# Optimization experiments

Hardware: AMD Instinct MI355X
Metric: run time of the kernel (lower is better)

The kernel has to match this reference:

```python
import jax, jax.numpy as jnp
from jax import lax
import numpy as np

B = 262144
CLASSES = 11


def setup_inputs() -> dict:
    key = jax.random.key(0)
    ks = jax.random.split(key, 8)
    exponents = jax.random.randint(ks[0], (B, 16), 0, CLASSES, dtype=jnp.int32)
    conv0_w = jax.random.normal(ks[1], (4, 12, 1, 2), jnp.float32) * 0.1
    conv0_b = jax.random.normal(ks[2], (4,), jnp.float32) * 0.05
    conv1_w = jax.random.normal(ks[3], (4, 12, 2, 1), jnp.float32) * 0.1
    # xavier-uniform linears, bias filled with 0.01 (as in init_weights)
    lim1 = float(np.sqrt(6.0 / (96 + 256)))
    linear_w = jax.random.uniform(ks[4], (256, 96), jnp.float32, -lim1, lim1)
    linear_b = jnp.full((256,), 0.01, jnp.float32)
    lim2 = float(np.sqrt(6.0 / (256 + 4)))
    out_w = jax.random.uniform(ks[5], (4, 256), jnp.float32, -lim2, lim2)
    out_b = jnp.full((4,), 0.01, jnp.float32)
    return {"exponents": exponents, "conv0_w": conv0_w, "conv0_b": conv0_b,
            "conv1_w": conv1_w, "linear_w": linear_w, "linear_b": linear_b,
            "out_w": out_w, "out_b": out_b}


def _conv(x, w):
    return lax.conv_general_dilated(x, w, (1, 1), 'VALID',
                                    dimension_numbers=('NCHW', 'OIHW', 'NCHW'))


def _forward(exponents, conv0_w, conv0_b, conv1_w, linear_w, linear_b, out_w, out_b):
    e = exponents.reshape(-1, 4, 4)
    # reconstruct board values: 0 tile stays 0, else 2**e
    x = jnp.where(e == 0, 0.0, jnp.exp2(e.astype(jnp.float32)))  # [B,4,4]
    # rotate_normalize: flips chosen from argmax corner (computed BEFORE flipping)
    corners = jnp.stack([x[:, 0, 0], x[:, 0, -1], x[:, -1, 0], x[:, -1, -1]], axis=1)
    ix = jnp.argmax(corners, axis=1)
    flip_v = ix >= 2          # floor(ix/2) == 1
    flip_h = (ix % 2) == 1
    x = jnp.where(flip_v[:, None, None], x[:, ::-1, :], x)
    x = jnp.where(flip_h[:, None, None], x[:, :, ::-1], x)
    # log2 with 0 -> 0, one-hot over 11 classes
    x_log = jnp.log2(x + (x == 0).astype(jnp.float32))
    onehot = jax.nn.one_hot(jnp.round(x_log).astype(jnp.int32), CLASSES,
                            dtype=jnp.float32)          # [B,4,4,11]
    onehot = jnp.transpose(onehot, (0, 3, 1, 2))         # [B,11,4,4]
    mask = onehot.sum(axis=1, keepdims=True)             # channel 0 (all ones)
    feat = jnp.concatenate([mask, onehot], axis=1)       # [B,12,4,4]
    zh = jax.nn.relu(_conv(feat, conv0_w) + conv0_b[None, :, None, None])  # [B,4,4,3]
    zv = jax.nn.relu(_conv(feat, conv1_w))                                  # [B,4,3,4]
    z1 = jnp.concatenate([zh.reshape(-1, 48), zv.reshape(-1, 48)], axis=1)  # [B,96]
    z2 = jax.nn.relu(z1 @ linear_w.T + linear_b)                            # [B,256]
    probs = jax.nn.softmax(z2 @ out_w.T + out_b, axis=1)                    # [B,4]
    # unscramble: vert swaps actions (0,1); horiz swaps actions (2,3)
    perm = jnp.stack([jnp.where(flip_v, 1, 0), jnp.where(flip_v, 0, 1),
                      jnp.where(flip_h, 3, 2), jnp.where(flip_h, 2, 3)], axis=1)
    return jnp.take_along_axis(probs, perm, axis=1)


def reference(exponents, conv0_w, conv0_b, conv1_w, linear_w, linear_b, out_w, out_b):
    return _forward(exponents, conv0_w, conv0_b, conv1_w, linear_w, linear_b, out_w, out_b)
```

## Files before the change

### kernel.cpp

```cpp
#include <hip/hip_runtime.h>

typedef unsigned int  u32;
typedef unsigned short u16;

typedef float    f4  __attribute__((ext_vector_type(4)));
typedef short    bf8 __attribute__((ext_vector_type(8)));
typedef __fp16   h8  __attribute__((ext_vector_type(8)));
typedef __fp16   h2  __attribute__((ext_vector_type(2)));

#define NBLK  1024
#define ITERS 4
#define ZSTR  104
#define SSTR  104

__device__ __forceinline__ u32 bfr(float f) {
    union { float f; u32 u; } v; v.f = f;
    return (v.u + 0x7fffu + ((v.u >> 16) & 1u)) >> 16;
}
__device__ __forceinline__ u32 pk2(float lo, float hi) { return bfr(lo) | (bfr(hi) << 16); }
__device__ __forceinline__ float blo(u32 u) { union { u32 u; float f; } v; v.u = u << 16;        return v.f; }
__device__ __forceinline__ float bhi(u32 u) { union { u32 u; float f; } v; v.u = u & 0xffff0000u; return v.f; }
__device__ __forceinline__ u32 pkh(float lo, float hi) {
    union { h2 h; u32 u; } v; v.h = __builtin_amdgcn_cvt_pkrtz(lo, hi); return v.u;
}
__device__ __forceinline__ u32 nrev(u32 x) {
    return ((x >> 12) & 0xFu) | ((x >> 4) & 0xF0u) | ((x << 4) & 0xF00u) | ((x << 12) & 0xF000u);
}

__launch_bounds__(256, 4)
__global__ void smartcnn_fused(const int* __restrict__ exps,
                               const float* __restrict__ c0w, const float* __restrict__ c0b,
                               const float* __restrict__ c1w,
                               const float* __restrict__ lw,  const float* __restrict__ lb,
                               const float* __restrict__ ow,  const float* __restrict__ ob,
                               float* __restrict__ out)
{
    __shared__ uint2  ThA[121];
    __shared__ uint2  TvA[121];
    __shared__ u16    z1[64 * ZSTR];
    __shared__ u32    zs[4][16 * SSTR / 2];
    __shared__ float4 Pbuf[4][4][16];
    __shared__ u32    flg[64];

    const int tid  = threadIdx.x;
    const int w    = tid >> 6;
    const int lane = tid & 63;
    const int m    = lane & 15;
    const int qd   = lane >> 4;

    for (int i = tid; i < 121; i += 256) {
        int v1 = i / 11, v2 = i - v1 * 11;
        float hv[4], vv[4];
        #pragma unroll
        for (int c = 0; c < 4; ++c) {
            hv[c] = fmaxf(c0w[c*24 + 0] + c0w[c*24 + (1+v1)*2 + 0] + c0b[c]
                        + c0w[c*24 + 1] + c0w[c*24 + (1+v2)*2 + 1], 0.f);
            vv[c] = fmaxf(c1w[c*24 + 0] + c1w[c*24 + (1+v1)*2 + 0]
                        + c1w[c*24 + 1] + c1w[c*24 + (1+v2)*2 + 1], 0.f);
        }
        ThA[i] = make_uint2(pk2(hv[0], hv[1]), pk2(hv[2], hv[3]));
        TvA[i] = make_uint2(pk2(vv[0], vv[1]), pk2(vv[2], vv[3]));
    }

    bf8 af[4][3];
    {
        u16* srow = (u16*)&zs[w][0] + m * SSTR;
        #pragma unroll
        for (int tt = 0; tt < 4; ++tt) {
            const float* rowp = lw + (size_t)((w*4 + tt)*16 + m)*96 + qd*24;
            #pragma unroll
            for (int v = 0; v < 6; ++v) {
                float4 x = *(const float4*)(rowp + v*4);
                u16 e[4] = {(u16)bfr(x.x), (u16)bfr(x.y), (u16)bfr(x.z), (u16)bfr(x.w)};
                #pragma unroll
                for (int j = 0; j < 4; ++j) {
                    int ko = qd*24 + v*4 + j;
                    int kp = (ko < 48) ? ((ko % 12)*4 + ko/12)
                                       : (48 + ((ko - 48) % 12)*4 + (ko - 48)/12);
                    srow[kp] = e[j];
                }
            }
            #pragma unroll
            for (int s = 0; s < 3; ++s)
                af[tt][s] = *(const bf8*)(srow + s*32 + qd*8);
        }
    }
    u32 owA[2][4];
    #pragma unroll
    for (int c = 0; c < 2; ++c) {
        int n8 = 64*w + 32*c + qd*8;
        #pragma unroll
        for (int k = 0; k < 4; ++k)
            owA[c][k] = (m < 4) ? pkh(ow[m*256 + n8 + 2*k], ow[m*256 + n8 + 2*k + 1]) : 0u;
    }
    u32 lbp[4][2];
    #pragma unroll
    for (int tt = 0; tt < 4; ++tt) {
        int n0 = 64*w + 16*tt + qd*4;
        lbp[tt][0] = pk2(lb[n0+0], lb[n0+1]);
        lbp[tt][1] = pk2(lb[n0+2], lb[n0+3]);
    }
    const float4 obv = *(const float4*)ob;

    const int b0 = blockIdx.x * (ITERS * 64);
    __syncthreads();

    int4 e4 = *(const int4*)(exps + (size_t)(b0 + w*16 + m)*16 + qd*4);
    u32 fl = 0;

    #pragma unroll 1
    for (int it = 0; it < ITERS; ++it) {
        if (it > 0) {
            float4 s0 = Pbuf[qd][0][m], s1 = Pbuf[qd][1][m];
            float4 s2 = Pbuf[qd][2][m], s3 = Pbuf[qd][3][m];
            float L0 = s0.x + s1.x + s2.x + s3.x + obv.x;
            float L1 = s0.y + s1.y + s2.y + s3.y + obv.y;
            float L2 = s0.z + s1.z + s2.z + s3.z + obv.z;
            float L3 = s0.w + s1.w + s2.w + s3.w + obv.w;
            float mx = fmaxf(fmaxf(L0, L1), fmaxf(L2, L3));
            float e0 = __expf(L0 - mx), e1 = __expf(L1 - mx), e2 = __expf(L2 - mx), e3 = __expf(L3 - mx);
            float inv = 1.0f / (e0 + e1 + e2 + e3);
            float p0 = e0 * inv, p1 = e1 * inv, p2 = e2 * inv, p3 = e3 * inv;
            float4 o;
            o.x = (fl & 1u) ? p1 : p0;
            o.y = (fl & 1u) ? p0 : p1;
            o.z = (fl & 2u) ? p3 : p2;
            o.w = (fl & 2u) ? p2 : p3;
            *(float4*)(out + (size_t)(b0 + (it-1)*64 + qd*16 + m) * 4) = o;
        }

        {
            u32 pkd = (u32)e4.x | ((u32)e4.y << 4) | ((u32)e4.z << 8) | ((u32)e4.w << 12);
            u32 R0 = (u32)__shfl((int)pkd, m);
            u32 R1 = (u32)__shfl((int)pkd, m + 16);
            u32 R2 = (u32)__shfl((int)pkd, m + 32);
            u32 R3 = (u32)__shfl((int)pkd, m + 48);
            u32 c0v = R0 & 15u, c1v = (R0 >> 12) & 15u, c2v = R3 & 15u, c3v = (R3 >> 12) & 15u;
            u32 best = c0v; int ix = 0;
            if (c1v > best) { best = c1v; ix = 1; }
            if (c2v > best) { best = c2v; ix = 2; }
            if (c3v > best) { best = c3v; ix = 3; }
            const bool fv = (ix >= 2), fh = ((ix & 1) != 0);
            u32 F[4];
            F[0] = fv ? R3 : R0;
            F[1] = fv ? R2 : R1;
            F[2] = fv ? R1 : R2;
            F[3] = fv ? R0 : R3;
            #pragma unroll
            for (int i = 0; i < 4; ++i) F[i] = fh ? nrev(F[i]) : F[i];

            if (qd == 0) flg[w*16 + m] = (u32)fv | ((u32)fh << 1);

            const u32 Fq = F[qd];
            u32 nbq[4], nbc[4];
            #pragma unroll
            for (int j = 0; j < 4; ++j) nbq[j] = (Fq >> (4*j)) & 15u;
            #pragma unroll
            for (int i = 0; i < 4; ++i) nbc[i] = (F[i] >> (4*qd)) & 15u;

            uint2 H0 = ThA[nbq[0]*11u + nbq[1]];
            uint2 H1 = ThA[nbq[1]*11u + nbq[2]];
            uint2 H2 = ThA[nbq[2]*11u + nbq[3]];
            uint2 V0 = TvA[nbc[0]*11u + nbc[1]];
            uint2 V1 = TvA[nbc[1]*11u + nbc[2]];
            uint2 V2 = TvA[nbc[2]*11u + nbc[3]];

            u16* zrow = &z1[(w*16 + m) * ZSTR];
            *(uint2*)(zrow + (qd*3 + 0)*4) = H0;
            *(uint2*)(zrow + (qd*3 + 1)*4) = H1;
            *(uint2*)(zrow + (qd*3 + 2)*4) = H2;
            *(uint2*)(zrow + 48 + (0*4 + qd)*4) = V0;
            *(uint2*)(zrow + 48 + (1*4 + qd)*4) = V1;
            *(uint2*)(zrow + 48 + (2*4 + qd)*4) = V2;
        }

        if (it + 1 < ITERS)
            e4 = *(const int4*)(exps + (size_t)(b0 + (it+1)*64 + w*16 + m)*16 + qd*4);

        __syncthreads();

        fl = flg[qd*16 + m];

        u32* zw = &zs[w][0];
        const int laneA = (((2*qd)    ) & 3)*16 + m;
        const int laneB = (((2*qd) + 1) & 3)*16 + m;
        #pragma unroll
        for (int G = 0; G < 4; ++G) {
            bf8 zb[3];
            #pragma unroll
            for (int s = 0; s < 3; ++s)
                zb[s] = *(const bf8*)(&z1[(G*16 + m)*ZSTR + s*32 + qd*8]);

            f4 acc_t[4];
            #pragma unroll
            for (int tt = 0; tt < 4; ++tt) {
                f4 b;
                b[0] = blo(lbp[tt][0]); b[1] = bhi(lbp[tt][0]);
                b[2] = blo(lbp[tt][1]); b[3] = bhi(lbp[tt][1]);
                acc_t[tt] = b;
            }
            #pragma unroll
            for (int s = 0; s < 3; ++s)
                #pragma unroll
                for (int tt = 0; tt < 4; ++tt)
                    acc_t[tt] = __builtin_amdgcn_mfma_f32_16x16x32_bf16(af[tt][s], zb[s], acc_t[tt], 0, 0, 0);

            u32 z2p[8];
            #pragma unroll
            for (int tt = 0; tt < 4; ++tt) {
                z2p[tt*2+0] = pkh(fmaxf(acc_t[tt][0], 0.f), fmaxf(acc_t[tt][1], 0.f));
                z2p[tt*2+1] = pkh(fmaxf(acc_t[tt][2], 0.f), fmaxf(acc_t[tt][3], 0.f));
            }
            *(uint4*)&zw[lane*12 + 0] = make_uint4(z2p[0], z2p[1], z2p[2], z2p[3]);
            *(uint4*)&zw[lane*12 + 4] = make_uint4(z2p[4], z2p[5], z2p[6], z2p[7]);

            f4 acc2 = {0.f, 0.f, 0.f, 0.f};
            #pragma unroll
            for (int c = 0; c < 2; ++c) {
                const int tt = 2*c + (qd >> 1);
                uint2 uA = *(const uint2*)&zw[laneA*12 + tt*2];
                uint2 uB = *(const uint2*)&zw[laneB*12 + tt*2];
                union { u32 u[4]; h8 v; } bu, au;
                bu.u[0] = uA.x; bu.u[1] = uA.y; bu.u[2] = uB.x; bu.u[3] = uB.y;
                au.u[0] = owA[c][0]; au.u[1] = owA[c][1]; au.u[2] = owA[c][2]; au.u[3] = owA[c][3];
                acc2 = __builtin_amdgcn_mfma_f32_16x16x32_f16(au.v, bu.v, acc2, 0, 0, 0);
            }
            if (qd == 0)
                Pbuf[G][w][m] = make_float4(acc2[0], acc2[1], acc2[2], acc2[3]);
        }
        __syncthreads();
    }

    {
        float4 s0 = Pbuf[qd][0][m], s1 = Pbuf[qd][1][m];
        float4 s2 = Pbuf[qd][2][m], s3 = Pbuf[qd][3][m];
        float L0 = s0.x + s1.x + s2.x + s3.x + obv.x;
        float L1 = s0.y + s1.y + s2.y + s3.y + obv.y;
        float L2 = s0.z + s1.z + s2.z + s3.z + obv.z;
        float L3 = s0.w + s1.w + s2.w + s3.w + obv.w;
        float mx = fmaxf(fmaxf(L0, L1), fmaxf(L2, L3));
        float e0 = __expf(L0 - mx), e1 = __expf(L1 - mx), e2 = __expf(L2 - mx), e3 = __expf(L3 - mx);
        float inv = 1.0f / (e0 + e1 + e2 + e3);
        float p0 = e0 * inv, p1 = e1 * inv, p2 = e2 * inv, p3 = e3 * inv;
        float4 o;
        o.x = (fl & 1u) ? p1 : p0;
        o.y = (fl & 1u) ? p0 : p1;
        o.z = (fl & 2u) ? p3 : p2;
        o.w = (fl & 2u) ? p2 : p3;
        *(float4*)(out + (size_t)(b0 + (ITERS-1)*64 + qd*16 + m) * 4) = o;
    }
}

extern "C" void kernel_launch(void* const* d_in, const int* in_sizes, int n_in,
                              void* d_out, int out_size, void* d_ws, size_t ws_size,
                              hipStream_t stream) {
    const int*   exps = (const int*)  d_in[0];
    const float* c0w  = (const float*)d_in[1];
    const float* c0b  = (const float*)d_in[2];
    const float* c1w  = (const float*)d_in[3];
    const float* lw   = (const float*)d_in[4];
    const float* lbv  = (const float*)d_in[5];
    const float* oww  = (const float*)d_in[6];
    const float* obv  = (const float*)d_in[7];
    smartcnn_fused<<<NBLK, 256, 0, stream>>>(exps, c0w, c0b, c1w, lw, lbv, oww, obv, (float*)d_out);
}
```

Baseline: 105.4 us.

## Switch to grid-stride chunk loop with 1280 blocks and fp32 bias init

Replaces the fixed four-chunks-per-block schedule with a grid-stride loop over 4096 chunks of 64 samples, launched as 1280 blocks, to change load balance across CUs and the tail. The second-layer bias is kept as fp32 float4 vectors instead of packed bf16 values that were unpacked on every iteration. Weight staging now reuses the z1 buffer and zs is resized. The 4096/1280 split leaves some blocks with one more chunk than others.

New measurement: 117.6 us. 11.6% more time.

```diff
diff --git a/kernel.cpp b/kernel.cpp
--- a/kernel.cpp
+++ b/kernel.cpp
@@ -8,18 +8,15 @@
 typedef __fp16   h8  __attribute__((ext_vector_type(8)));
 typedef __fp16   h2  __attribute__((ext_vector_type(2)));
 
-#define NBLK  1024
-#define ITERS 4
-#define ZSTR  104
-#define SSTR  104
+#define NBLK   1280
+#define NCHUNK 4096
+#define ZSTR   104
 
 __device__ __forceinline__ u32 bfr(float f) {
     union { float f; u32 u; } v; v.f = f;
     return (v.u + 0x7fffu + ((v.u >> 16) & 1u)) >> 16;
 }
 __device__ __forceinline__ u32 pk2(float lo, float hi) { return bfr(lo) | (bfr(hi) << 16); }
-__device__ __forceinline__ float blo(u32 u) { union { u32 u; float f; } v; v.u = u << 16;        return v.f; }
-__device__ __forceinline__ float bhi(u32 u) { union { u32 u; float f; } v; v.u = u & 0xffff0000u; return v.f; }
 __device__ __forceinline__ u32 pkh(float lo, float hi) {
     union { h2 h; u32 u; } v; v.h = __builtin_amdgcn_cvt_pkrtz(lo, hi); return v.u;
 }
@@ -38,7 +35,7 @@
     __shared__ uint2  ThA[121];
     __shared__ uint2  TvA[121];
     __shared__ u16    z1[64 * ZSTR];
-    __shared__ u32    zs[4][16 * SSTR / 2];
+    __shared__ u32    zs[4][64 * 12];
     __shared__ float4 Pbuf[4][4][16];
     __shared__ u32    flg[64];
 
@@ -64,7 +61,7 @@
 
     bf8 af[4][3];
     {
-        u16* srow = (u16*)&zs[w][0] + m * SSTR;
+        u16* srow = &z1[(w*16 + m) * ZSTR];
         #pragma unroll
         for (int tt = 0; tt < 4; ++tt) {
             const float* rowp = lw + (size_t)((w*4 + tt)*16 + m)*96 + qd*24;
@@ -93,24 +90,24 @@
         for (int k = 0; k < 4; ++k)
             owA[c][k] = (m < 4) ? pkh(ow[m*256 + n8 + 2*k], ow[m*256 + n8 + 2*k + 1]) : 0u;
     }
-    u32 lbp[4][2];
+    f4 lb4[4];
     #pragma unroll
-    for (int tt = 0; tt < 4; ++tt) {
-        int n0 = 64*w + 16*tt + qd*4;
-        lbp[tt][0] = pk2(lb[n0+0], lb[n0+1]);
-        lbp[tt][1] = pk2(lb[n0+2], lb[n0+3]);
-    }
+    for (int tt = 0; tt < 4; ++tt)
+        lb4[tt] = *(const f4*)(lb + 64*w + 16*tt + qd*4);
     const float4 obv = *(const float4*)ob;
 
-    const int b0 = blockIdx.x * (ITERS * 64);
     __syncthreads();
 
-    int4 e4 = *(const int4*)(exps + (size_t)(b0 + w*16 + m)*16 + qd*4);
+    int bi = blockIdx.x;
+    int4 e4 = *(const int4*)(exps + (size_t)(bi*64 + w*16 + m)*16 + qd*4);
     u32 fl = 0;
+    int pb = -1;
 
     #pragma unroll 1
-    for (int it = 0; it < ITERS; ++it) {
-        if (it > 0) {
+    for (; bi < NCHUNK; bi += NBLK) {
+        const int b0 = bi * 64;
+
+        if (pb >= 0) {
             float4 s0 = Pbuf[qd][0][m], s1 = Pbuf[qd][1][m];
             float4 s2 = Pbuf[qd][2][m], s3 = Pbuf[qd][3][m];
             float L0 = s0.x + s1.x + s2.x + s3.x + obv.x;
@@ -126,7 +123,7 @@
             o.y = (fl & 1u) ? p0 : p1;
             o.z = (fl & 2u) ? p3 : p2;
             o.w = (fl & 2u) ? p2 : p3;
-            *(float4*)(out + (size_t)(b0 + (it-1)*64 + qd*16 + m) * 4) = o;
+            *(float4*)(out + (size_t)(pb + qd*16 + m) * 4) = o;
         }
 
         {
@@ -174,12 +171,13 @@
             *(uint2*)(zrow + 48 + (2*4 + qd)*4) = V2;
         }
 
-        if (it + 1 < ITERS)
-            e4 = *(const int4*)(exps + (size_t)(b0 + (it+1)*64 + w*16 + m)*16 + qd*4);
+        if (bi + NBLK < NCHUNK)
+            e4 = *(const int4*)(exps + (size_t)((bi + NBLK)*64 + w*16 + m)*16 + qd*4);
 
         __syncthreads();
 
         fl = flg[qd*16 + m];
+        pb = b0;
 
         u32* zw = &zs[w][0];
         const int laneA = (((2*qd)    ) & 3)*16 + m;
@@ -191,14 +189,7 @@
             for (int s = 0; s < 3; ++s)
                 zb[s] = *(const bf8*)(&z1[(G*16 + m)*ZSTR + s*32 + qd*8]);
 
-            f4 acc_t[4];
-            #pragma unroll
-            for (int tt = 0; tt < 4; ++tt) {
-                f4 b;
-                b[0] = blo(lbp[tt][0]); b[1] = bhi(lbp[tt][0]);
-                b[2] = blo(lbp[tt][1]); b[3] = bhi(lbp[tt][1]);
-                acc_t[tt] = b;
-            }
+            f4 acc_t[4] = {lb4[0], lb4[1], lb4[2], lb4[3]};
             #pragma unroll
             for (int s = 0; s < 3; ++s)
                 #pragma unroll
@@ -231,7 +222,7 @@
         __syncthreads();
     }
 
-    {
+    if (pb >= 0) {
         float4 s0 = Pbuf[qd][0][m], s1 = Pbuf[qd][1][m];
         float4 s2 = Pbuf[qd][2][m], s3 = Pbuf[qd][3][m];
         float L0 = s0.x + s1.x + s2.x + s3.x + obv.x;
@@ -247,7 +238,7 @@
         o.y = (fl & 1u) ? p0 : p1;
         o.z = (fl & 2u) ? p3 : p2;
         o.w = (fl & 2u) ? p2 : p3;
-        *(float4*)(out + (size_t)(b0 + (ITERS-1)*64 + qd*16 + m) * 4) = o;
+        *(float4*)(out + (size_t)(pb + qd*16 + m) * 4) = o;
     }
 }
 
```

## Permute linear weight rows so MFMA outputs feed second MFMA directly in registers

Applied to the files above, without the earlier changes.

The order of the linear-layer output features assigned to each MFMA tile is permuted, both for the weight rows and for the bias. With that order, the accumulator layout of the first bf16 MFMA matches the operand layout the second f16 MFMA expects. This removes the per-group shared-memory round trip (write z2, read it back through lane shuffles) and the separate zs scratch buffer, and the bias is kept as fp32 vectors instead of bf16-packed values. It relies on the permuted feature order lining up exactly with the output-weight packing.

Result: no change. 104.0 us (-1.3%).

```diff
diff --git a/kernel.cpp b/kernel.cpp
--- a/kernel.cpp
+++ b/kernel.cpp
@@ -11,15 +11,12 @@
 #define NBLK  1024
 #define ITERS 4
 #define ZSTR  104
-#define SSTR  104
 
 __device__ __forceinline__ u32 bfr(float f) {
     union { float f; u32 u; } v; v.f = f;
     return (v.u + 0x7fffu + ((v.u >> 16) & 1u)) >> 16;
 }
 __device__ __forceinline__ u32 pk2(float lo, float hi) { return bfr(lo) | (bfr(hi) << 16); }
-__device__ __forceinline__ float blo(u32 u) { union { u32 u; float f; } v; v.u = u << 16;        return v.f; }
-__device__ __forceinline__ float bhi(u32 u) { union { u32 u; float f; } v; v.u = u & 0xffff0000u; return v.f; }
 __device__ __forceinline__ u32 pkh(float lo, float hi) {
     union { h2 h; u32 u; } v; v.h = __builtin_amdgcn_cvt_pkrtz(lo, hi); return v.u;
 }
@@ -38,7 +35,6 @@
     __shared__ uint2  ThA[121];
     __shared__ uint2  TvA[121];
     __shared__ u16    z1[64 * ZSTR];
-    __shared__ u32    zs[4][16 * SSTR / 2];
     __shared__ float4 Pbuf[4][4][16];
     __shared__ u32    flg[64];
 
@@ -48,6 +44,7 @@
     const int m    = lane & 15;
     const int qd   = lane >> 4;
 
+
     for (int i = tid; i < 121; i += 256) {
         int v1 = i / 11, v2 = i - v1 * 11;
         float hv[4], vv[4];
@@ -64,10 +61,12 @@
 
     bf8 af[4][3];
     {
-        u16* srow = (u16*)&zs[w][0] + m * SSTR;
+        u16* srow = &z1[(w*16 + m) * ZSTR];
         #pragma unroll
         for (int tt = 0; tt < 4; ++tt) {
-            const float* rowp = lw + (size_t)((w*4 + tt)*16 + m)*96 + qd*24;
+            const int tbase = ((tt & 1) ? 4 : 0) + ((tt >> 1) ? 32 : 0);
+            const int fid = 64*w + tbase + 8*(m >> 2) + (m & 3);
+            const float* rowp = lw + (size_t)fid*96 + qd*24;
             #pragma unroll
             for (int v = 0; v < 6; ++v) {
                 float4 x = *(const float4*)(rowp + v*4);
@@ -93,12 +92,11 @@
         for (int k = 0; k < 4; ++k)
             owA[c][k] = (m < 4) ? pkh(ow[m*256 + n8 + 2*k], ow[m*256 + n8 + 2*k + 1]) : 0u;
     }
-    u32 lbp[4][2];
+    f4 lb4[4];
     #pragma unroll
     for (int tt = 0; tt < 4; ++tt) {
-        int n0 = 64*w + 16*tt + qd*4;
-        lbp[tt][0] = pk2(lb[n0+0], lb[n0+1]);
-        lbp[tt][1] = pk2(lb[n0+2], lb[n0+3]);
+        const int tbase = ((tt & 1) ? 4 : 0) + ((tt >> 1) ? 32 : 0);
+        lb4[tt] = *(const f4*)(lb + 64*w + tbase + 8*qd);
     }
     const float4 obv = *(const float4*)ob;
 
@@ -181,9 +179,6 @@
 
         fl = flg[qd*16 + m];
 
-        u32* zw = &zs[w][0];
-        const int laneA = (((2*qd)    ) & 3)*16 + m;
-        const int laneB = (((2*qd) + 1) & 3)*16 + m;
         #pragma unroll
         for (int G = 0; G < 4; ++G) {
             bf8 zb[3];
@@ -191,37 +186,21 @@
             for (int s = 0; s < 3; ++s)
                 zb[s] = *(const bf8*)(&z1[(G*16 + m)*ZSTR + s*32 + qd*8]);
 
-            f4 acc_t[4];
-            #pragma unroll
-            for (int tt = 0; tt < 4; ++tt) {
-                f4 b;
-                b[0] = blo(lbp[tt][0]); b[1] = bhi(lbp[tt][0]);
-                b[2] = blo(lbp[tt][1]); b[3] = bhi(lbp[tt][1]);
-                acc_t[tt] = b;
-            }
+            f4 acc_t[4] = {lb4[0], lb4[1], lb4[2], lb4[3]};
             #pragma unroll
             for (int s = 0; s < 3; ++s)
                 #pragma unroll
                 for (int tt = 0; tt < 4; ++tt)
                     acc_t[tt] = __builtin_amdgcn_mfma_f32_16x16x32_bf16(af[tt][s], zb[s], acc_t[tt], 0, 0, 0);
 
-            u32 z2p[8];
-            #pragma unroll
-            for (int tt = 0; tt < 4; ++tt) {
-                z2p[tt*2+0] = pkh(fmaxf(acc_t[tt][0], 0.f), fmaxf(acc_t[tt][1], 0.f));
-                z2p[tt*2+1] = pkh(fmaxf(acc_t[tt][2], 0.f), fmaxf(acc_t[tt][3], 0.f));
-            }
-            *(uint4*)&zw[lane*12 + 0] = make_uint4(z2p[0], z2p[1], z2p[2], z2p[3]);
-            *(uint4*)&zw[lane*12 + 4] = make_uint4(z2p[4], z2p[5], z2p[6], z2p[7]);
-
             f4 acc2 = {0.f, 0.f, 0.f, 0.f};
             #pragma unroll
             for (int c = 0; c < 2; ++c) {
-                const int tt = 2*c + (qd >> 1);
-                uint2 uA = *(const uint2*)&zw[laneA*12 + tt*2];
-                uint2 uB = *(const uint2*)&zw[laneB*12 + tt*2];
                 union { u32 u[4]; h8 v; } bu, au;
-                bu.u[0] = uA.x; bu.u[1] = uA.y; bu.u[2] = uB.x; bu.u[3] = uB.y;
+                bu.u[0] = pkh(fmaxf(acc_t[2*c  ][0], 0.f), fmaxf(acc_t[2*c  ][1], 0.f));
+                bu.u[1] = pkh(fmaxf(acc_t[2*c  ][2], 0.f), fmaxf(acc_t[2*c  ][3], 0.f));
+                bu.u[2] = pkh(fmaxf(acc_t[2*c+1][0], 0.f), fmaxf(acc_t[2*c+1][1], 0.f));
+                bu.u[3] = pkh(fmaxf(acc_t[2*c+1][2], 0.f), fmaxf(acc_t[2*c+1][3], 0.f));
                 au.u[0] = owA[c][0]; au.u[1] = owA[c][1]; au.u[2] = owA[c][2]; au.u[3] = owA[c][3];
                 acc2 = __builtin_amdgcn_mfma_f32_16x16x32_f16(au.v, bu.v, acc2, 0, 0, 0);
             }
```
